# Performance work log

Measured on AMD Instinct MI355X. Metric: run time of the kernel, lower is better.

## Reference

```python
import jax, jax.numpy as jnp
import numpy as np

N_NODES = 100000
N_EDGES = 1000000
N_GRAPHS = 128
IN_DIM, HID, LAT, N_LAYERS = 32, 64, 32, 3


def setup_inputs() -> dict:
    key = jax.random.key(0)
    ks = jax.random.split(key, 10)
    x = jax.random.normal(ks[0], (N_NODES, IN_DIM), dtype=jnp.float32)
    edge_index = jax.random.randint(ks[1], (2, N_EDGES), 0, N_NODES, dtype=jnp.int64)
    batch = jnp.sort(jax.random.randint(ks[2], (N_NODES,), 0, N_GRAPHS, dtype=jnp.int64))
    s_in = 1.0 / np.sqrt(IN_DIM)
    s_h = 1.0 / np.sqrt(HID)
    return {
        "x": x,
        "edge_index": edge_index,
        "batch": batch,
        "w_in": jax.random.normal(ks[3], (IN_DIM, HID), dtype=jnp.float32) * s_in,
        "b_in": jnp.zeros((HID,), jnp.float32),
        "w1": jax.random.normal(ks[4], (N_LAYERS, HID, HID), dtype=jnp.float32) * s_h,
        "b1": jnp.zeros((N_LAYERS, HID), jnp.float32),
        "w2": jax.random.normal(ks[5], (N_LAYERS, HID, HID), dtype=jnp.float32) * s_h,
        "b2": jnp.zeros((N_LAYERS, HID), jnp.float32),
        "w_fc": jax.random.normal(ks[6], (HID, LAT), dtype=jnp.float32) * s_h,
        "b_fc": jnp.zeros((LAT,), jnp.float32),
    }


def reference(x, edge_index, batch, w_in, b_in, w1, b1, w2, b2, w_fc, b_fc):
    # Input projection: [N, in] -> [N, H]
    h = x @ w_in + b_in
    src, dst = edge_index[0], edge_index[1]
    for i in range(N_LAYERS):
        h_skip = h
        # GINConv (eps=0): aggregate neighbor sum then MLP
        agg = jax.ops.segment_sum(h[src], dst, num_segments=N_NODES)  # [N, H]
        m = h + agg
        m = jax.nn.relu(m @ w1[i] + b1[i])
        m = jax.nn.relu(m @ w2[i] + b2[i])
        # dropout is identity in eval mode; residual skip
        h = m + h_skip
    # global_add_pool over graphs
    pooled = jax.ops.segment_sum(h, batch, num_segments=N_GRAPHS)  # [G, H]
    return pooled @ w_fc + b_fc
```

## Files before the change

kernel.cpp:

```cpp
#include <hip/hip_runtime.h>

#define N_NODES 100000
#define N_EDGES 1000000
#define N_GRAPHS 128
#define IN_DIM 32
#define HID 64
#define LAT 32
#define N_LAYERS 3

#define MPAD 68

#define BSZ 256
#define NBK ((N_NODES + BSZ - 1) / BSZ)
#define EPB 4096
#define NBIN_BLOCKS ((N_EDGES + EPB - 1) / EPB)

__global__ __launch_bounds__(256) void proj_kernel(
    const float* __restrict__ x, const float* __restrict__ w_in,
    const float* __restrict__ b_in, float* __restrict__ h) {
    __shared__ float ws[IN_DIM * HID];
    __shared__ float xs[4 * IN_DIM];
    int tid = threadIdx.x;
    for (int i = tid; i < IN_DIM * HID / 4; i += 256)
        ((float4*)ws)[i] = ((const float4*)w_in)[i];
    if (tid < 32) {
        int r = tid >> 3, c4 = tid & 7;
        int nn = blockIdx.x * 4 + r;
        float4 v = make_float4(0.f, 0.f, 0.f, 0.f);
        if (nn < N_NODES) v = ((const float4*)(x + (size_t)nn * IN_DIM))[c4];
        ((float4*)xs)[tid] = v;
    }
    __syncthreads();
    int w = tid >> 6, j = tid & 63;
    int n = blockIdx.x * 4 + w;
    if (n >= N_NODES) return;
    float acc = b_in[j];
#pragma unroll
    for (int k = 0; k < IN_DIM; k += 4) {
        float4 xv = *(const float4*)&xs[w * IN_DIM + k];
        acc += xv.x * ws[(k + 0) * HID + j];
        acc += xv.y * ws[(k + 1) * HID + j];
        acc += xv.z * ws[(k + 2) * HID + j];
        acc += xv.w * ws[(k + 3) * HID + j];
    }
    h[(size_t)n * HID + j] = acc;
}

__global__ __launch_bounds__(256) void bhist_kernel(const int* __restrict__ ei,
                                                    int* __restrict__ bhist) {
    __shared__ int hs[NBK];
    for (int i = threadIdx.x; i < NBK; i += 256) hs[i] = 0;
    __syncthreads();
    int e = blockIdx.x * (256 * 16) + threadIdx.x;
#pragma unroll
    for (int k = 0; k < 16; k++, e += 256)
        if (e < N_EDGES) atomicAdd(&hs[ei[N_EDGES + e] >> 8], 1);
    __syncthreads();
    for (int i = threadIdx.x; i < NBK; i += 256) {
        int c = hs[i];
        if (c) atomicAdd(&bhist[i], c);
    }
}

__global__ __launch_bounds__(512) void bscan_kernel(const int* __restrict__ bhist,
                                                    int* __restrict__ bstart,
                                                    int* __restrict__ bcursor) {
    __shared__ int sc[512];
    int tid = threadIdx.x;
    int v = (tid < NBK) ? bhist[tid] : 0;
    sc[tid] = v;
    __syncthreads();
    for (int off = 1; off < 512; off <<= 1) {
        int t = (tid >= off) ? sc[tid - off] : 0;
        __syncthreads();
        sc[tid] += t;
        __syncthreads();
    }
    if (tid < NBK) {
        int ex = sc[tid] - v;
        bstart[tid] = ex;
        bcursor[tid] = ex;
    }
    if (tid == 0) bstart[NBK] = N_EDGES;
}

__global__ __launch_bounds__(512) void binsort_kernel(const int* __restrict__ ei,
                                                      int* __restrict__ bcursor,
                                                      int* __restrict__ tmp) {
    __shared__ int hist[NBK];
    __shared__ int lofs[NBK + 1];
    __shared__ int cur[NBK];
    __shared__ int gbase[NBK];
    __shared__ int sc[512];
    __shared__ int stage[EPB];
    int tid = threadIdx.x;
    int e0 = blockIdx.x * EPB;
    int nE = min(EPB, N_EDGES - e0);
    for (int i = tid; i < NBK; i += 512) hist[i] = 0;
    __syncthreads();
    for (int i = tid; i < nE; i += 512)
        atomicAdd(&hist[ei[N_EDGES + e0 + i] >> 8], 1);
    __syncthreads();
    int v = (tid < NBK) ? hist[tid] : 0;
    sc[tid] = v;
    __syncthreads();
    for (int off = 1; off < 512; off <<= 1) {
        int t = (tid >= off) ? sc[tid - off] : 0;
        __syncthreads();
        sc[tid] += t;
        __syncthreads();
    }
    if (tid < NBK) {
        int ex = sc[tid] - v;
        lofs[tid] = ex;
        cur[tid] = ex;
        gbase[tid] = atomicAdd(&bcursor[tid], v);
    }
    if (tid == 0) lofs[NBK] = nE;
    __syncthreads();
    for (int i = tid; i < nE; i += 512) {
        int s = ei[e0 + i];
        int d = ei[N_EDGES + e0 + i];
        int b = d >> 8;
        int p = atomicAdd(&cur[b], 1);
        stage[p] = ((d & 255) << 17) | s;
    }
    __syncthreads();
    for (int i = tid; i < nE; i += 512) {
        int pv = stage[i];
        int lo = 0, hi = NBK;
        while (hi - lo > 1) {
            int mid = (lo + hi) >> 1;
            if (lofs[mid] <= i) lo = mid; else hi = mid;
        }
        tmp[gbase[lo] + (i - lofs[lo])] = pv;
    }
}

__global__ __launch_bounds__(256) void csr_finalize_kernel(
    const int* __restrict__ bstart, const int* __restrict__ tmp,
    int* __restrict__ srcs, int* __restrict__ offsets) {
    __shared__ int cnt[BSZ];
    __shared__ int ofs[BSZ];
    __shared__ int cur[BSZ];
    int b = blockIdx.x, tid = threadIdx.x;
    int beg = bstart[b], end = bstart[b + 1];
    cnt[tid] = 0;
    __syncthreads();
    for (int i = beg + tid; i < end; i += 256)
        atomicAdd(&cnt[tmp[i] >> 17], 1);
    __syncthreads();
    int v = cnt[tid];
    ofs[tid] = v;
    __syncthreads();
    for (int off = 1; off < 256; off <<= 1) {
        int t = (tid >= off) ? ofs[tid - off] : 0;
        __syncthreads();
        ofs[tid] += t;
        __syncthreads();
    }
    int ex = ofs[tid] - v;
    cur[tid] = ex;
    int n = b * BSZ + tid;
    if (n < N_NODES) {
        offsets[n] = beg + ex;
        if (n == N_NODES - 1) offsets[N_NODES] = beg + ex + v;
    }
    __syncthreads();
    for (int i = beg + tid; i < end; i += 256) {
        int pv = tmp[i];
        int p = atomicAdd(&cur[pv >> 17], 1);
        srcs[beg + p] = pv & 0x1FFFF;
    }
}

__global__ __launch_bounds__(256) void gather_kernel(
    const int* __restrict__ offsets, const int* __restrict__ srcs,
    const float* __restrict__ h, float* __restrict__ agg) {
    int w = threadIdx.x >> 6, j = threadIdx.x & 63;
    int n = blockIdx.x * 4 + w;
    if (n >= N_NODES) return;
    int beg = offsets[n], end = offsets[n + 1];
    float acc0 = 0.f, acc1 = 0.f, acc2 = 0.f, acc3 = 0.f;
    for (int c = beg; c < end; c += 64) {
        int myS = (c + j < end) ? srcs[c + j] : 0;
        int m = min(64, end - c);
        int i = 0;
        for (; i + 3 < m; i += 4) {
            int s0 = __shfl(myS, i);
            int s1 = __shfl(myS, i + 1);
            int s2 = __shfl(myS, i + 2);
            int s3 = __shfl(myS, i + 3);
            acc0 += h[(size_t)s0 * HID + j];
            acc1 += h[(size_t)s1 * HID + j];
            acc2 += h[(size_t)s2 * HID + j];
            acc3 += h[(size_t)s3 * HID + j];
        }
        for (; i < m; i++) acc0 += h[(size_t)__shfl(myS, i) * HID + j];
    }
    agg[(size_t)n * HID + j] = acc0 + acc1 + acc2 + acc3;
}

__global__ __launch_bounds__(512) void mlp_kernel(
    float* __restrict__ h, const float* __restrict__ agg,
    const float* __restrict__ w1, const float* __restrict__ b1,
    const float* __restrict__ w2, const float* __restrict__ b2) {
    __shared__ float w1s[HID * HID];
    __shared__ float w2s[HID * HID];
    __shared__ float ms[64 * MPAD];
    int tid = threadIdx.x;
    int row0 = blockIdx.x * 64;
    for (int i = tid; i < HID * HID / 4; i += 512) {
        ((float4*)w1s)[i] = ((const float4*)w1)[i];
        ((float4*)w2s)[i] = ((const float4*)w2)[i];
    }
#pragma unroll
    for (int i = 0; i < 2; i++) {
        int f = tid + i * 512;
        int r = f >> 4, c4 = f & 15;
        int n = row0 + r;
        float4 mv = make_float4(0.f, 0.f, 0.f, 0.f);
        if (n < N_NODES) {
            float4 h4 = ((const float4*)(h + (size_t)n * HID))[c4];
            float4 a4 = ((const float4*)(agg + (size_t)n * HID))[c4];
            mv = make_float4(h4.x + a4.x, h4.y + a4.y, h4.z + a4.z, h4.w + a4.w);
        }
        *(float4*)&ms[r * MPAD + c4 * 4] = mv;
    }
    __syncthreads();

    int ty = tid >> 4, tx = tid & 15;
    int r0 = ty * 2, c0 = tx * 4;

    float4 a0, a1;
#define GEMM_LDS(WS)                                                          \
    do {                                                                      \
        a0 = make_float4(0.f, 0.f, 0.f, 0.f); a1 = a0;                        \
        _Pragma("unroll 4")                                                   \
        for (int k0 = 0; k0 < HID; k0 += 4) {                                 \
            float4 m0 = *(const float4*)&ms[(r0 + 0) * MPAD + k0];            \
            float4 m1 = *(const float4*)&ms[(r0 + 1) * MPAD + k0];            \
            float4 w0 = *(const float4*)&WS[(k0 + 0) * HID + c0];             \
            float4 w1v = *(const float4*)&WS[(k0 + 1) * HID + c0];            \
            float4 w2v = *(const float4*)&WS[(k0 + 2) * HID + c0];            \
            float4 w3v = *(const float4*)&WS[(k0 + 3) * HID + c0];            \
            a0.x += m0.x * w0.x + m0.y * w1v.x + m0.z * w2v.x + m0.w * w3v.x; \
            a0.y += m0.x * w0.y + m0.y * w1v.y + m0.z * w2v.y + m0.w * w3v.y; \
            a0.z += m0.x * w0.z + m0.y * w1v.z + m0.z * w2v.z + m0.w * w3v.z; \
            a0.w += m0.x * w0.w + m0.y * w1v.w + m0.z * w2v.w + m0.w * w3v.w; \
            a1.x += m1.x * w0.x + m1.y * w1v.x + m1.z * w2v.x + m1.w * w3v.x; \
            a1.y += m1.x * w0.y + m1.y * w1v.y + m1.z * w2v.y + m1.w * w3v.y; \
            a1.z += m1.x * w0.z + m1.y * w1v.z + m1.z * w2v.z + m1.w * w3v.z; \
            a1.w += m1.x * w0.w + m1.y * w1v.w + m1.z * w2v.w + m1.w * w3v.w; \
        }                                                                     \
    } while (0)

    GEMM_LDS(w1s);

    float4 bv1 = *(const float4*)&b1[c0];
    float4 t0 = make_float4(fmaxf(a0.x + bv1.x, 0.f), fmaxf(a0.y + bv1.y, 0.f),
                            fmaxf(a0.z + bv1.z, 0.f), fmaxf(a0.w + bv1.w, 0.f));
    float4 t1 = make_float4(fmaxf(a1.x + bv1.x, 0.f), fmaxf(a1.y + bv1.y, 0.f),
                            fmaxf(a1.z + bv1.z, 0.f), fmaxf(a1.w + bv1.w, 0.f));

    __syncthreads();
    *(float4*)&ms[(r0 + 0) * MPAD + c0] = t0;
    *(float4*)&ms[(r0 + 1) * MPAD + c0] = t1;
    __syncthreads();

    GEMM_LDS(w2s);

    float4 bv2 = *(const float4*)&b2[c0];
#pragma unroll
    for (int i = 0; i < 2; i++) {
        int n = row0 + r0 + i;
        if (n < N_NODES) {
            float4 av = (i == 0) ? a0 : a1;
            float4 hold = *(const float4*)(h + (size_t)n * HID + c0);
            float4 o;
            o.x = fmaxf(av.x + bv2.x, 0.f) + hold.x;
            o.y = fmaxf(av.y + bv2.y, 0.f) + hold.y;
            o.z = fmaxf(av.z + bv2.z, 0.f) + hold.z;
            o.w = fmaxf(av.w + bv2.w, 0.f) + hold.w;
            *(float4*)(h + (size_t)n * HID + c0) = o;
        }
    }
#undef GEMM_LDS
}

__global__ __launch_bounds__(256) void pool_kernel(
    const float* __restrict__ h, const int* __restrict__ batch,
    float* __restrict__ pooled) {
    int tid = threadIdx.x;
    int w = tid >> 6, j = tid & 63;
    int n0 = blockIdx.x * 256 + w * 64;
    if (n0 >= N_NODES) return;
    int nend = min(n0 + 64, N_NODES);
    float acc = 0.f;
    int cur = batch[n0];
    for (int n = n0; n < nend; n++) {
        int b = batch[n];
        if (b != cur) {
            atomicAdd(&pooled[cur * HID + j], acc);
            acc = 0.f;
            cur = b;
        }
        acc += h[(size_t)n * HID + j];
    }
    atomicAdd(&pooled[cur * HID + j], acc);
}

__global__ __launch_bounds__(256) void final_kernel(
    const float* __restrict__ pooled, const float* __restrict__ w_fc,
    const float* __restrict__ b_fc, float* __restrict__ out) {
    int gid = blockIdx.x * 256 + threadIdx.x;
    if (gid >= N_GRAPHS * LAT) return;
    int g = gid >> 5, j = gid & 31;
    float acc = b_fc[j];
#pragma unroll
    for (int k = 0; k < HID; k++)
        acc += pooled[g * HID + k] * w_fc[k * LAT + j];
    out[gid] = acc;
}

extern "C" void kernel_launch(void* const* d_in, const int* in_sizes, int n_in,
                              void* d_out, int out_size, void* d_ws,
                              size_t ws_size, hipStream_t stream) {
    const float* x     = (const float*)d_in[0];
    const int*   ei    = (const int*)d_in[1];
    const int*   batch = (const int*)d_in[2];
    const float* w_in  = (const float*)d_in[3];
    const float* b_in  = (const float*)d_in[4];
    const float* w1    = (const float*)d_in[5];
    const float* b1    = (const float*)d_in[6];
    const float* w2    = (const float*)d_in[7];
    const float* b2    = (const float*)d_in[8];
    const float* w_fc  = (const float*)d_in[9];
    const float* b_fc  = (const float*)d_in[10];
    float* out = (float*)d_out;

    float* h       = (float*)d_ws;
    float* agg     = h + (size_t)N_NODES * HID;
    float* pooled  = agg + (size_t)N_NODES * HID;
    int*   offsets = (int*)(pooled + N_GRAPHS * HID);
    int*   srcs    = offsets + (N_NODES + 2);
    int* tmp     = (int*)agg;
    int* bhist   = tmp + N_EDGES;
    int* bstart  = bhist + NBK;
    int* bcursor = bstart + (NBK + 1);

    proj_kernel<<<(N_NODES + 3) / 4, 256, 0, stream>>>(x, w_in, b_in, h);

    hipMemsetAsync(bhist, 0, NBK * sizeof(int), stream);
    bhist_kernel<<<(N_EDGES + 4095) / 4096, 256, 0, stream>>>(ei, bhist);
    bscan_kernel<<<1, 512, 0, stream>>>(bhist, bstart, bcursor);
    binsort_kernel<<<NBIN_BLOCKS, 512, 0, stream>>>(ei, bcursor, tmp);
    csr_finalize_kernel<<<NBK, 256, 0, stream>>>(bstart, tmp, srcs, offsets);

    for (int i = 0; i < N_LAYERS; i++) {
        gather_kernel<<<(N_NODES + 3) / 4, 256, 0, stream>>>(offsets, srcs, h, agg);
        mlp_kernel<<<(N_NODES + 63) / 64, 512, 0, stream>>>(
            h, agg, w1 + (size_t)i * HID * HID, b1 + (size_t)i * HID,
            w2 + (size_t)i * HID * HID, b2 + (size_t)i * HID);
    }

    hipMemsetAsync(pooled, 0, N_GRAPHS * HID * sizeof(float), stream);
    pool_kernel<<<(N_NODES + 255) / 256, 256, 0, stream>>>(h, batch, pooled);
    final_kernel<<<(N_GRAPHS * LAT + 255) / 256, 256, 0, stream>>>(
        pooled, w_fc, b_fc, out);
}
```

Before: 414.7 us.

## Fuse neighbor gather into GIN MLP kernel with ping-pong h buffers

Merges the per-layer gather and MLP kernels into one kernel. Each of the 8 wavefronts in a block aggregates the neighbors of 8 rows straight into shared memory, and the two-layer MLP then runs on that tile. Ping-pong h buffers avoid read-write hazards across blocks. This removes the agg array write and re-read and one launch per layer, but the gather now runs inside 512-thread blocks that hold 40KB+ of shared memory, which may reduce occupancy and latency hiding for the random gathers.

```diff
diff --git a/kernel.cpp b/kernel.cpp
--- a/kernel.cpp
+++ b/kernel.cpp
@@ -174,35 +174,9 @@
     }
 }
 
-__global__ __launch_bounds__(256) void gather_kernel(
+__global__ __launch_bounds__(512) void gin_layer_kernel(
+    const float* __restrict__ hin, float* __restrict__ hout,
     const int* __restrict__ offsets, const int* __restrict__ srcs,
-    const float* __restrict__ h, float* __restrict__ agg) {
-    int w = threadIdx.x >> 6, j = threadIdx.x & 63;
-    int n = blockIdx.x * 4 + w;
-    if (n >= N_NODES) return;
-    int beg = offsets[n], end = offsets[n + 1];
-    float acc0 = 0.f, acc1 = 0.f, acc2 = 0.f, acc3 = 0.f;
-    for (int c = beg; c < end; c += 64) {
-        int myS = (c + j < end) ? srcs[c + j] : 0;
-        int m = min(64, end - c);
-        int i = 0;
-        for (; i + 3 < m; i += 4) {
-            int s0 = __shfl(myS, i);
-            int s1 = __shfl(myS, i + 1);
-            int s2 = __shfl(myS, i + 2);
-            int s3 = __shfl(myS, i + 3);
-            acc0 += h[(size_t)s0 * HID + j];
-            acc1 += h[(size_t)s1 * HID + j];
-            acc2 += h[(size_t)s2 * HID + j];
-            acc3 += h[(size_t)s3 * HID + j];
-        }
-        for (; i < m; i++) acc0 += h[(size_t)__shfl(myS, i) * HID + j];
-    }
-    agg[(size_t)n * HID + j] = acc0 + acc1 + acc2 + acc3;
-}
-
-__global__ __launch_bounds__(512) void mlp_kernel(
-    float* __restrict__ h, const float* __restrict__ agg,
     const float* __restrict__ w1, const float* __restrict__ b1,
     const float* __restrict__ w2, const float* __restrict__ b2) {
     __shared__ float w1s[HID * HID];
@@ -214,18 +188,34 @@
         ((float4*)w1s)[i] = ((const float4*)w1)[i];
         ((float4*)w2s)[i] = ((const float4*)w2)[i];
     }
-#pragma unroll
-    for (int i = 0; i < 2; i++) {
-        int f = tid + i * 512;
-        int r = f >> 4, c4 = f & 15;
+
+    int w = tid >> 6, j = tid & 63;
+#pragma unroll 1
+    for (int r = w * 8; r < w * 8 + 8; r++) {
         int n = row0 + r;
-        float4 mv = make_float4(0.f, 0.f, 0.f, 0.f);
+        float acc0 = 0.f, acc1 = 0.f, acc2 = 0.f, acc3 = 0.f;
+        float hv = 0.f;
         if (n < N_NODES) {
-            float4 h4 = ((const float4*)(h + (size_t)n * HID))[c4];
-            float4 a4 = ((const float4*)(agg + (size_t)n * HID))[c4];
-            mv = make_float4(h4.x + a4.x, h4.y + a4.y, h4.z + a4.z, h4.w + a4.w);
+            hv = hin[(size_t)n * HID + j];
+            int beg = offsets[n], end = offsets[n + 1];
+            for (int c = beg; c < end; c += 64) {
+                int myS = (c + j < end) ? srcs[c + j] : 0;
+                int m = min(64, end - c);
+                int i = 0;
+                for (; i + 3 < m; i += 4) {
+                    int s0 = __shfl(myS, i);
+                    int s1 = __shfl(myS, i + 1);
+                    int s2 = __shfl(myS, i + 2);
+                    int s3 = __shfl(myS, i + 3);
+                    acc0 += hin[(size_t)s0 * HID + j];
+                    acc1 += hin[(size_t)s1 * HID + j];
+                    acc2 += hin[(size_t)s2 * HID + j];
+                    acc3 += hin[(size_t)s3 * HID + j];
+                }
+                for (; i < m; i++) acc0 += hin[(size_t)__shfl(myS, i) * HID + j];
+            }
         }
-        *(float4*)&ms[r * MPAD + c4 * 4] = mv;
+        ms[r * MPAD + j] = hv + acc0 + acc1 + acc2 + acc3;
     }
     __syncthreads();
 
@@ -276,13 +266,13 @@
         int n = row0 + r0 + i;
         if (n < N_NODES) {
             float4 av = (i == 0) ? a0 : a1;
-            float4 hold = *(const float4*)(h + (size_t)n * HID + c0);
+            float4 hold = *(const float4*)(hin + (size_t)n * HID + c0);
             float4 o;
             o.x = fmaxf(av.x + bv2.x, 0.f) + hold.x;
             o.y = fmaxf(av.y + bv2.y, 0.f) + hold.y;
             o.z = fmaxf(av.z + bv2.z, 0.f) + hold.z;
             o.w = fmaxf(av.w + bv2.w, 0.f) + hold.w;
-            *(float4*)(h + (size_t)n * HID + c0) = o;
+            *(float4*)(hout + (size_t)n * HID + c0) = o;
         }
     }
 #undef GEMM_LDS
@@ -340,11 +330,11 @@
     float* out = (float*)d_out;
 
     float* h       = (float*)d_ws;
-    float* agg     = h + (size_t)N_NODES * HID;
-    float* pooled  = agg + (size_t)N_NODES * HID;
+    float* h2      = h + (size_t)N_NODES * HID;
+    float* pooled  = h2 + (size_t)N_NODES * HID;
     int*   offsets = (int*)(pooled + N_GRAPHS * HID);
     int*   srcs    = offsets + (N_NODES + 2);
-    int* tmp     = (int*)agg;
+    int* tmp     = (int*)h2;
     int* bhist   = tmp + N_EDGES;
     int* bstart  = bhist + NBK;
     int* bcursor = bstart + (NBK + 1);
@@ -357,15 +347,18 @@
     binsort_kernel<<<NBIN_BLOCKS, 512, 0, stream>>>(ei, bcursor, tmp);
     csr_finalize_kernel<<<NBK, 256, 0, stream>>>(bstart, tmp, srcs, offsets);
 
+    float* hin = h;
+    float* hout = h2;
     for (int i = 0; i < N_LAYERS; i++) {
-        gather_kernel<<<(N_NODES + 3) / 4, 256, 0, stream>>>(offsets, srcs, h, agg);
-        mlp_kernel<<<(N_NODES + 63) / 64, 512, 0, stream>>>(
-            h, agg, w1 + (size_t)i * HID * HID, b1 + (size_t)i * HID,
-            w2 + (size_t)i * HID * HID, b2 + (size_t)i * HID);
+        gin_layer_kernel<<<(N_NODES + 63) / 64, 512, 0, stream>>>(
+            hin, hout, offsets, srcs, w1 + (size_t)i * HID * HID,
+            b1 + (size_t)i * HID, w2 + (size_t)i * HID * HID,
+            b2 + (size_t)i * HID);
+        float* t = hin; hin = hout; hout = t;
     }
 
     hipMemsetAsync(pooled, 0, N_GRAPHS * HID * sizeof(float), stream);
-    pool_kernel<<<(N_NODES + 255) / 256, 256, 0, stream>>>(h, batch, pooled);
+    pool_kernel<<<(N_NODES + 255) / 256, 256, 0, stream>>>(hin, batch, pooled);
     final_kernel<<<(N_GRAPHS * LAT + 255) / 256, 256, 0, stream>>>(
         pooled, w_fc, b_fc, out);
 }
```

New measurement: 470.2 us. 13.4% more time.
